# Kernel optimization log

Hardware: AMD Instinct MI355X
Metric: run time of the kernel (lower is better)

Reference implementation:

```python
import jax, jax.numpy as jnp
import numpy as np

N_NODES = 100000
N_EDGES = 1600000
IN_DIM = 64
OUT_DIM = 64
HIDDEN = 64  # fixed in edge_weight_mlp
POS_DIM = 3


def setup_inputs() -> dict:
    key = jax.random.key(0)
    ks = jax.random.split(key, 10)
    x = jax.random.normal(ks[0], (N_NODES, IN_DIM), dtype=jnp.float32)
    edge_index = jax.random.randint(ks[1], (2, N_EDGES), 0, N_NODES, dtype=jnp.int64)
    pos = jax.random.normal(ks[2], (N_NODES, POS_DIM), dtype=jnp.float32)
    # edge_weight_mlp params: Linear(2*IN_DIM+1 -> 64), Linear(64 -> 1)
    s1 = 1.0 / np.sqrt(2 * IN_DIM + 1)
    w1 = jax.random.uniform(ks[3], (2 * IN_DIM + 1, HIDDEN), jnp.float32, -s1, s1)
    b1 = jax.random.uniform(ks[4], (HIDDEN,), jnp.float32, -s1, s1)
    s2 = 1.0 / np.sqrt(HIDDEN)
    w2 = jax.random.uniform(ks[5], (HIDDEN, 1), jnp.float32, -s2, s2)
    b2 = jax.random.uniform(ks[6], (1,), jnp.float32, -s2, s2)
    # transform: Linear(IN_DIM -> OUT_DIM)
    st = 1.0 / np.sqrt(IN_DIM)
    wt = jax.random.uniform(ks[7], (IN_DIM, OUT_DIM), jnp.float32, -st, st)
    bt = jax.random.uniform(ks[8], (OUT_DIM,), jnp.float32, -st, st)
    return {"x": x, "edge_index": edge_index, "pos": pos,
            "w1": w1, "b1": b1, "w2": w2, "b2": b2, "wt": wt, "bt": bt}


def reference(x, edge_index, pos, w1, b1, w2, b2, wt, bt):
    src, dst = edge_index[0], edge_index[1]
    # edge weights: MLP on [x_src, x_dst, |pos_dst - pos_src|]
    edge_length = jnp.linalg.norm(pos[dst] - pos[src], axis=1, keepdims=True)  # [E,1]
    edge_feat = jnp.concatenate([x[src], x[dst], edge_length], axis=1)  # [E, 2*in+1]
    h = jax.nn.relu(edge_feat @ w1 + b1)
    edge_weights = jax.nn.sigmoid(h @ w2 + b2)  # [E,1]
    # node transform, gather, weight, scatter-add
    x_t = x @ wt + bt  # [N, out]
    messages = x_t[src] * edge_weights  # [E, out]
    out = jax.ops.segment_sum(messages, dst, num_segments=x.shape[0])  # [N, out]
    return out, edge_weights
```

## Files before the change

### kernel.cpp

```cpp
#include <hip/hip_runtime.h>
#include <hip/hip_bf16.h>
#include <math.h>

#define NN 100000
#define NE 1600000
#define CAP 48
#define NB 391
#define BCAP 4608
#define EPB 4096
#define NBLKA ((NE + EPB - 1) / EPB)
#define PSTR 72

typedef __attribute__((ext_vector_type(8))) short short8;
typedef __attribute__((ext_vector_type(4))) float floatx4;

static __device__ __forceinline__ unsigned short f2bb(float f) {
    __hip_bfloat16 h = __float2bfloat16(f);
    return *(unsigned short*)&h;
}

__global__ __launch_bounds__(256) void prep_mfma(
    const float* __restrict__ x, const float* __restrict__ w1,
    const float* __restrict__ b1, const float* __restrict__ pos,
    unsigned int* __restrict__ rec, unsigned short* __restrict__ hd,
    float4* __restrict__ pos4) {
    __shared__ unsigned short As[64 * PSTR];
    __shared__ unsigned short Bs[128 * PSTR];
    int t = threadIdx.x;
    int nbase = blockIdx.x * 64;
    {
        int r = t & 63;
        int node = nbase + r; if (node >= NN) node = NN - 1;
        const float4* xr = (const float4*)(x + (size_t)node * 64);
#pragma unroll
        for (int i = 0; i < 4; ++i) {
            int s = (t >> 6) + 4 * i;
            float4 v = xr[s];
            ushort4 o = {f2bb(v.x), f2bb(v.y), f2bb(v.z), f2bb(v.w)};
            *(ushort4*)&As[r * PSTR + s * 4] = o;
        }
    }
    {
        int n = t & 127;
        int kh = t >> 7;
        int krow = (n < 64) ? 0 : 64;
        int col = n & 63;
#pragma unroll
        for (int i = 0; i < 32; ++i) {
            int k = kh * 32 + i;
            Bs[n * PSTR + k] = f2bb(w1[(krow + k) * 64 + col]);
        }
    }
    if (t < 64) {
        int node = nbase + t;
        if (node < NN)
            pos4[node] = make_float4(pos[node * 3 + 0], pos[node * 3 + 1],
                                     pos[node * 3 + 2], 0.f);
    }
    __syncthreads();
    int lane = t & 63, wave = t >> 6;
    int grp = lane >> 4, l15 = lane & 15;
    floatx4 acc[8] = {};
    int arow = wave * 16 + l15;
#pragma unroll
    for (int ks = 0; ks < 2; ++ks) {
        int koff = ks * 32 + grp * 8;
        short8 a = *(const short8*)&As[arow * PSTR + koff];
#pragma unroll
        for (int nt = 0; nt < 8; ++nt) {
            short8 b = *(const short8*)&Bs[(nt * 16 + l15) * PSTR + koff];
            acc[nt] = __builtin_amdgcn_mfma_f32_16x16x32_bf16(a, b, acc[nt], 0, 0, 0);
        }
    }
#pragma unroll
    for (int nt = 0; nt < 8; ++nt) {
#pragma unroll
        for (int r = 0; r < 4; ++r) {
            int nr = wave * 16 + grp * 4 + r;
            int node = nbase + nr;
            if (node >= NN) continue;
            if (nt < 4) {
                int col = nt * 16 + l15;
                unsigned xbits = As[nr * PSTR + col];
                rec[(size_t)node * 64 + col] =
                    ((unsigned)f2bb(acc[nt][r]) << 16) | xbits;
            } else {
                int col = (nt - 4) * 16 + l15;
                hd[(size_t)node * 64 + col] = f2bb(acc[nt][r] + b1[col]);
            }
        }
    }
}

__global__ __launch_bounds__(256) void bucket_kernel(
    const int* __restrict__ ei, int* __restrict__ gcursor,
    uint2* __restrict__ bucketed) {
    __shared__ int cnt[NB];
    __shared__ int base_s[NB];
    int t = threadIdx.x;
    for (int i = t; i < NB; i += 256) cnt[i] = 0;
    __syncthreads();
    int e0 = blockIdx.x * EPB;
    unsigned int tags[16];
    int srcs[16], dsts[16];
#pragma unroll
    for (int i = 0; i < 16; ++i) {
        int e = e0 + i * 256 + t;
        tags[i] = 0xFFFFFFFFu;
        if (e < NE) {
            srcs[i] = ei[e];
            dsts[i] = ei[NE + e];
            int b = dsts[i] >> 8;
            int slot = atomicAdd(&cnt[b], 1);
            tags[i] = ((unsigned)b << 12) | (unsigned)slot;
        }
    }
    __syncthreads();
    for (int b = t; b < NB; b += 256)
        base_s[b] = atomicAdd(&gcursor[b], cnt[b]);
    __syncthreads();
#pragma unroll
    for (int i = 0; i < 16; ++i) {
        if (tags[i] != 0xFFFFFFFFu) {
            int e = e0 + i * 256 + t;
            int b = (int)(tags[i] >> 12);
            int slot = (int)(tags[i] & 0xFFFu);
            int pos = base_s[b] + slot;
            if (pos < BCAP) {
                bucketed[(size_t)b * BCAP + pos] =
                    make_uint2((unsigned)srcs[i] | (((unsigned)dsts[i] & 255u) << 17),
                               (unsigned)e);
            }
        }
    }
}

__global__ __launch_bounds__(1024) void csr_kernel(
    const uint2* __restrict__ bucketed, const int* __restrict__ gcursor,
    uint2* __restrict__ pairs, int* __restrict__ deg) {
    __shared__ int cur[256];
    int t = threadIdx.x;
    if (t < 256) cur[t] = 0;
    __syncthreads();
    int b = blockIdx.x;
    int n0 = b << 8;
    int cnt = gcursor[b];
    if (cnt > BCAP) cnt = BCAP;
    for (int i = t; i < cnt; i += 1024) {
        uint2 en = bucketed[(size_t)b * BCAP + i];
        int dwb = (int)((en.x >> 17) & 255u);
        unsigned src = en.x & 0x1FFFFu;
        int slot = atomicAdd(&cur[dwb], 1);
        if (slot < CAP)
            pairs[(size_t)(n0 + dwb) * CAP + slot] = make_uint2(src, en.y);
    }
    __syncthreads();
    if (t < 256) {
        int node = n0 + t;
        if (node < NN) deg[node] = (cur[t] > CAP) ? CAP : cur[t];
    }
}

__global__ __launch_bounds__(256) void mega_kernel(
    const uint2* __restrict__ pairs, const int* __restrict__ deg,
    const unsigned int* __restrict__ rec, const unsigned short* __restrict__ hd,
    const float4* __restrict__ pos4, const float* __restrict__ w1,
    const float* __restrict__ w2, const float* __restrict__ b2,
    float* __restrict__ ew_out, unsigned short* __restrict__ aggb,
    float* __restrict__ sumw) {
    int t = threadIdx.x;
    int w = t >> 6, lane = t & 63;
    int e4 = lane >> 4, hg = lane & 15;
    int node = blockIdx.x * 4 + w;
    if (node >= NN) return;

    float acc0 = 0.f, acc1 = 0.f, acc2 = 0.f, acc3 = 0.f, sw = 0.f;
    int d = deg[node];
    uint2 hz = ((const uint2*)(hd + (size_t)node * 64))[hg];
    float zb0 = __uint_as_float(hz.x << 16);
    float zb1 = __uint_as_float(hz.x & 0xFFFF0000u);
    float zb2 = __uint_as_float(hz.y << 16);
    float zb3 = __uint_as_float(hz.y & 0xFFFF0000u);
    float4 w24 = ((const float4*)w2)[hg];
    float4 wl4 = ((const float4*)(w1 + 128 * 64))[hg];
    float4 pd = pos4[node];
    float b2v = b2[0];
    const uint2* seg = pairs + (size_t)node * CAP;

    if (d > 0) {
        int i0 = (e4 < d) ? e4 : (d - 1);
        uint2 pr_c = seg[i0];
        int i1 = (4 + e4 < d) ? (4 + e4) : (d - 1);
        uint2 pr_n = (4 < d) ? seg[i1] : pr_c;
        uint4 u_c = ((const uint4*)rec)[(size_t)pr_c.x * 16 + hg];
        float4 ps_c = pos4[pr_c.x];

        for (int j = 0; j < d; j += 4) {
            int jn = j + 4;
            uint2 pr_n2 = pr_n;
            uint4 u_n = u_c;
            float4 ps_n = ps_c;
            if (jn < d) {
                u_n = ((const uint4*)rec)[(size_t)pr_n.x * 16 + hg];
                ps_n = pos4[pr_n.x];
                int i2 = (jn + 4 + e4 < d) ? (jn + 4 + e4) : (d - 1);
                if (jn + 4 < d) pr_n2 = seg[i2];
            }
            bool valid = (j + e4 < d);
            float dx = pd.x - ps_c.x;
            float dy = pd.y - ps_c.y;
            float dz = pd.z - ps_c.z;
            float len = __builtin_amdgcn_sqrtf(dx * dx + dy * dy + dz * dz);

            float z0 = zb0 + __uint_as_float(u_c.x & 0xFFFF0000u) + len * wl4.x;
            float z1 = zb1 + __uint_as_float(u_c.y & 0xFFFF0000u) + len * wl4.y;
            float z2 = zb2 + __uint_as_float(u_c.z & 0xFFFF0000u) + len * wl4.z;
            float z3 = zb3 + __uint_as_float(u_c.w & 0xFFFF0000u) + len * wl4.w;
            float tt = fmaxf(z0, 0.f) * w24.x;
            tt = fmaf(fmaxf(z1, 0.f), w24.y, tt);
            tt = fmaf(fmaxf(z2, 0.f), w24.z, tt);
            tt = fmaf(fmaxf(z3, 0.f), w24.w, tt);
            tt += __shfl_xor(tt, 1);
            tt += __shfl_xor(tt, 2);
            tt += __shfl_xor(tt, 4);
            tt += __shfl_xor(tt, 8);
            float ew = __builtin_amdgcn_rcpf(1.f + __expf(-(tt + b2v)));
            if (valid) {
                if (hg == 0) ew_out[pr_c.y] = ew;
                acc0 = fmaf(ew, __uint_as_float(u_c.x << 16), acc0);
                acc1 = fmaf(ew, __uint_as_float(u_c.y << 16), acc1);
                acc2 = fmaf(ew, __uint_as_float(u_c.z << 16), acc2);
                acc3 = fmaf(ew, __uint_as_float(u_c.w << 16), acc3);
                sw += ew;
            }
            pr_c = pr_n; pr_n = pr_n2; u_c = u_n; ps_c = ps_n;
        }
    }
#pragma unroll
    for (int off = 16; off < 64; off <<= 1) {
        acc0 += __shfl_xor(acc0, off);
        acc1 += __shfl_xor(acc1, off);
        acc2 += __shfl_xor(acc2, off);
        acc3 += __shfl_xor(acc3, off);
        sw   += __shfl_xor(sw, off);
    }
    if (e4 == 0) {
        ushort4 o = {f2bb(acc0), f2bb(acc1), f2bb(acc2), f2bb(acc3)};
        *(ushort4*)(aggb + (size_t)node * 64 + hg * 4) = o;
    }
    if (lane == 0) sumw[node] = sw;
}

__global__ __launch_bounds__(256) void transform_mfma(
    const unsigned short* __restrict__ aggb, const float* __restrict__ sumw,
    const float* __restrict__ wt, const float* __restrict__ bt,
    float* __restrict__ out) {
    __shared__ unsigned short As[64 * PSTR];
    __shared__ unsigned short Bs[64 * PSTR];
    int t = threadIdx.x;
    int nbase = blockIdx.x * 64;
    {
        int r = t & 63;
        int node = nbase + r; if (node >= NN) node = NN - 1;
        const uint4* ar = (const uint4*)(aggb + (size_t)node * 64);
#pragma unroll
        for (int i = 0; i < 2; ++i) {
            int s = (t >> 6) + 4 * i;
            *(uint4*)&As[r * PSTR + s * 8] = ar[s];
        }
    }
    {
        int n = t & 63;
        int kq = t >> 6;
#pragma unroll
        for (int i = 0; i < 16; ++i) {
            int k = kq * 16 + i;
            Bs[n * PSTR + k] = f2bb(wt[k * 64 + n]);
        }
    }
    __syncthreads();
    int lane = t & 63, wave = t >> 6;
    int grp = lane >> 4, l15 = lane & 15;
    floatx4 acc[4] = {};
    int arow = wave * 16 + l15;
#pragma unroll
    for (int ks = 0; ks < 2; ++ks) {
        int koff = ks * 32 + grp * 8;
        short8 a = *(const short8*)&As[arow * PSTR + koff];
#pragma unroll
        for (int nt = 0; nt < 4; ++nt) {
            short8 b = *(const short8*)&Bs[(nt * 16 + l15) * PSTR + koff];
            acc[nt] = __builtin_amdgcn_mfma_f32_16x16x32_bf16(a, b, acc[nt], 0, 0, 0);
        }
    }
#pragma unroll
    for (int nt = 0; nt < 4; ++nt) {
        int col = nt * 16 + l15;
        float btv = bt[col];
#pragma unroll
        for (int r = 0; r < 4; ++r) {
            int node = nbase + wave * 16 + grp * 4 + r;
            if (node < NN)
                out[(size_t)node * 64 + col] = acc[nt][r] + sumw[node] * btv;
        }
    }
}

extern "C" void kernel_launch(void* const* d_in, const int* in_sizes, int n_in,
                              void* d_out, int out_size, void* d_ws, size_t ws_size,
                              hipStream_t stream) {
    const float* x   = (const float*)d_in[0];
    const int*   ei  = (const int*)d_in[1];
    const float* pos = (const float*)d_in[2];
    const float* w1  = (const float*)d_in[3];
    const float* b1  = (const float*)d_in[4];
    const float* w2  = (const float*)d_in[5];
    const float* b2  = (const float*)d_in[6];
    const float* wt  = (const float*)d_in[7];
    const float* bt  = (const float*)d_in[8];

    float* out    = (float*)d_out;
    float* ew_out = out + (size_t)NN * 64;

    unsigned int* rec = (unsigned int*)d_ws;
    unsigned short* hd = (unsigned short*)(rec + (size_t)NN * 64);
    uint2* pairs = (uint2*)(hd + (size_t)NN * 64);
    unsigned short* aggb = (unsigned short*)(pairs + (size_t)NN * CAP);
    float4* pos4 = (float4*)(aggb + (size_t)NN * 64);
    float* sumw = (float*)(pos4 + NN);
    int* gcursor = (int*)(sumw + NN);
    int* deg = gcursor + NB;

    uint2* bucketed = (uint2*)d_out;

    hipMemsetAsync(gcursor, 0, NB * sizeof(int), stream);
    prep_mfma<<<(NN + 63) / 64, 256, 0, stream>>>(x, w1, b1, pos, rec, hd, pos4);
    bucket_kernel<<<NBLKA, 256, 0, stream>>>(ei, gcursor, bucketed);
    csr_kernel<<<NB, 1024, 0, stream>>>(bucketed, gcursor, pairs, deg);
    mega_kernel<<<(NN + 3) / 4, 256, 0, stream>>>(pairs, deg, rec, hd, pos4,
                                                  w1, w2, b2, ew_out, aggb, sumw);
    transform_mfma<<<(NN + 63) / 64, 256, 0, stream>>>(aggb, sumw, wt, bt, out);
}
```

Baseline: 259.3 us.

## Fuse prep and bucket kernels; process 8 edges per wave in mega kernel

Merges the node-prep MFMA kernel and the edge-bucketing kernel into one launch, with block index choosing the role and a shared LDS buffer, so the two independent phases can overlap and one launch is removed. Separately, the mega kernel now handles 8 edges per wave step with 8 lanes per edge, each lane owning 8 features. This halves the loop trip count and cuts one shuffle stage from the per-edge reduction. The cost is more registers per lane, and lanes go idle when a node's degree is not a multiple of 8.

```diff
diff --git a/kernel.cpp b/kernel.cpp
--- a/kernel.cpp
+++ b/kernel.cpp
@@ -9,6 +9,7 @@
 #define BCAP 4608
 #define EPB 4096
 #define NBLKA ((NE + EPB - 1) / EPB)
+#define NPREP ((NN + 63) / 64)
 #define PSTR 72
 
 typedef __attribute__((ext_vector_type(8))) short short8;
@@ -18,118 +19,125 @@
     __hip_bfloat16 h = __float2bfloat16(f);
     return *(unsigned short*)&h;
 }
-
-__global__ __launch_bounds__(256) void prep_mfma(
+static __device__ __forceinline__ float hi_f(unsigned u) {
+    return __uint_as_float(u & 0xFFFF0000u);
+}
+static __device__ __forceinline__ float lo_f(unsigned u) {
+    return __uint_as_float(u << 16);
+}
+
+__global__ __launch_bounds__(256) void fused_prep_bucket(
     const float* __restrict__ x, const float* __restrict__ w1,
     const float* __restrict__ b1, const float* __restrict__ pos,
+    const int* __restrict__ ei,
     unsigned int* __restrict__ rec, unsigned short* __restrict__ hd,
-    float4* __restrict__ pos4) {
-    __shared__ unsigned short As[64 * PSTR];
-    __shared__ unsigned short Bs[128 * PSTR];
+    float4* __restrict__ pos4, int* __restrict__ gcursor,
+    uint2* __restrict__ bucketed) {
+    __shared__ __align__(16) unsigned char smem[(64 + 128) * PSTR * 2];
     int t = threadIdx.x;
-    int nbase = blockIdx.x * 64;
-    {
-        int r = t & 63;
-        int node = nbase + r; if (node >= NN) node = NN - 1;
-        const float4* xr = (const float4*)(x + (size_t)node * 64);
-#pragma unroll
-        for (int i = 0; i < 4; ++i) {
-            int s = (t >> 6) + 4 * i;
-            float4 v = xr[s];
-            ushort4 o = {f2bb(v.x), f2bb(v.y), f2bb(v.z), f2bb(v.w)};
-            *(ushort4*)&As[r * PSTR + s * 4] = o;
-        }
-    }
-    {
-        int n = t & 127;
-        int kh = t >> 7;
-        int krow = (n < 64) ? 0 : 64;
-        int col = n & 63;
-#pragma unroll
-        for (int i = 0; i < 32; ++i) {
-            int k = kh * 32 + i;
-            Bs[n * PSTR + k] = f2bb(w1[(krow + k) * 64 + col]);
-        }
-    }
-    if (t < 64) {
-        int node = nbase + t;
-        if (node < NN)
-            pos4[node] = make_float4(pos[node * 3 + 0], pos[node * 3 + 1],
-                                     pos[node * 3 + 2], 0.f);
-    }
-    __syncthreads();
-    int lane = t & 63, wave = t >> 6;
-    int grp = lane >> 4, l15 = lane & 15;
-    floatx4 acc[8] = {};
-    int arow = wave * 16 + l15;
-#pragma unroll
-    for (int ks = 0; ks < 2; ++ks) {
-        int koff = ks * 32 + grp * 8;
-        short8 a = *(const short8*)&As[arow * PSTR + koff];
+    if (blockIdx.x < NPREP) {
+        unsigned short* As = (unsigned short*)smem;
+        unsigned short* Bs = As + 64 * PSTR;
+        int nbase = blockIdx.x * 64;
+        {
+            int r = t & 63;
+            int node = nbase + r; if (node >= NN) node = NN - 1;
+            const float4* xr = (const float4*)(x + (size_t)node * 64);
+#pragma unroll
+            for (int i = 0; i < 4; ++i) {
+                int s = (t >> 6) + 4 * i;
+                float4 v = xr[s];
+                ushort4 o = {f2bb(v.x), f2bb(v.y), f2bb(v.z), f2bb(v.w)};
+                *(ushort4*)&As[r * PSTR + s * 4] = o;
+            }
+        }
+        {
+            int n = t & 127;
+            int kh = t >> 7;
+            int krow = (n < 64) ? 0 : 64;
+            int col = n & 63;
+#pragma unroll
+            for (int i = 0; i < 32; ++i) {
+                int k = kh * 32 + i;
+                Bs[n * PSTR + k] = f2bb(w1[(krow + k) * 64 + col]);
+            }
+        }
+        if (t < 64) {
+            int node = nbase + t;
+            if (node < NN)
+                pos4[node] = make_float4(pos[node * 3 + 0], pos[node * 3 + 1],
+                                         pos[node * 3 + 2], 0.f);
+        }
+        __syncthreads();
+        int lane = t & 63, wave = t >> 6;
+        int grp = lane >> 4, l15 = lane & 15;
+        floatx4 acc[8] = {};
+        int arow = wave * 16 + l15;
+#pragma unroll
+        for (int ks = 0; ks < 2; ++ks) {
+            int koff = ks * 32 + grp * 8;
+            short8 a = *(const short8*)&As[arow * PSTR + koff];
+#pragma unroll
+            for (int nt = 0; nt < 8; ++nt) {
+                short8 b = *(const short8*)&Bs[(nt * 16 + l15) * PSTR + koff];
+                acc[nt] = __builtin_amdgcn_mfma_f32_16x16x32_bf16(a, b, acc[nt], 0, 0, 0);
+            }
+        }
 #pragma unroll
         for (int nt = 0; nt < 8; ++nt) {
-            short8 b = *(const short8*)&Bs[(nt * 16 + l15) * PSTR + koff];
-            acc[nt] = __builtin_amdgcn_mfma_f32_16x16x32_bf16(a, b, acc[nt], 0, 0, 0);
-        }
-    }
-#pragma unroll
-    for (int nt = 0; nt < 8; ++nt) {
-#pragma unroll
-        for (int r = 0; r < 4; ++r) {
-            int nr = wave * 16 + grp * 4 + r;
-            int node = nbase + nr;
-            if (node >= NN) continue;
-            if (nt < 4) {
-                int col = nt * 16 + l15;
-                unsigned xbits = As[nr * PSTR + col];
-                rec[(size_t)node * 64 + col] =
-                    ((unsigned)f2bb(acc[nt][r]) << 16) | xbits;
-            } else {
-                int col = (nt - 4) * 16 + l15;
-                hd[(size_t)node * 64 + col] = f2bb(acc[nt][r] + b1[col]);
-            }
-        }
-    }
-}
-
-__global__ __launch_bounds__(256) void bucket_kernel(
-    const int* __restrict__ ei, int* __restrict__ gcursor,
-    uint2* __restrict__ bucketed) {
-    __shared__ int cnt[NB];
-    __shared__ int base_s[NB];
-    int t = threadIdx.x;
-    for (int i = t; i < NB; i += 256) cnt[i] = 0;
-    __syncthreads();
-    int e0 = blockIdx.x * EPB;
-    unsigned int tags[16];
-    int srcs[16], dsts[16];
-#pragma unroll
-    for (int i = 0; i < 16; ++i) {
-        int e = e0 + i * 256 + t;
-        tags[i] = 0xFFFFFFFFu;
-        if (e < NE) {
-            srcs[i] = ei[e];
-            dsts[i] = ei[NE + e];
-            int b = dsts[i] >> 8;
-            int slot = atomicAdd(&cnt[b], 1);
-            tags[i] = ((unsigned)b << 12) | (unsigned)slot;
-        }
-    }
-    __syncthreads();
-    for (int b = t; b < NB; b += 256)
-        base_s[b] = atomicAdd(&gcursor[b], cnt[b]);
-    __syncthreads();
-#pragma unroll
-    for (int i = 0; i < 16; ++i) {
-        if (tags[i] != 0xFFFFFFFFu) {
+#pragma unroll
+            for (int r = 0; r < 4; ++r) {
+                int nr = wave * 16 + grp * 4 + r;
+                int node = nbase + nr;
+                if (node >= NN) continue;
+                if (nt < 4) {
+                    int col = nt * 16 + l15;
+                    unsigned xbits = As[nr * PSTR + col];
+                    rec[(size_t)node * 64 + col] =
+                        ((unsigned)f2bb(acc[nt][r]) << 16) | xbits;
+                } else {
+                    int col = (nt - 4) * 16 + l15;
+                    hd[(size_t)node * 64 + col] = f2bb(acc[nt][r] + b1[col]);
+                }
+            }
+        }
+    } else {
+        int* cnt = (int*)smem;
+        int* base_s = cnt + NB;
+        for (int i = t; i < NB; i += 256) cnt[i] = 0;
+        __syncthreads();
+        int e0 = (blockIdx.x - NPREP) * EPB;
+        unsigned int tags[16];
+        int srcs[16], dsts[16];
+#pragma unroll
+        for (int i = 0; i < 16; ++i) {
             int e = e0 + i * 256 + t;
-            int b = (int)(tags[i] >> 12);
-            int slot = (int)(tags[i] & 0xFFFu);
-            int pos = base_s[b] + slot;
-            if (pos < BCAP) {
-                bucketed[(size_t)b * BCAP + pos] =
-                    make_uint2((unsigned)srcs[i] | (((unsigned)dsts[i] & 255u) << 17),
-                               (unsigned)e);
+            tags[i] = 0xFFFFFFFFu;
+            if (e < NE) {
+                srcs[i] = ei[e];
+                dsts[i] = ei[NE + e];
+                int b = dsts[i] >> 8;
+                int slot = atomicAdd(&cnt[b], 1);
+                tags[i] = ((unsigned)b << 12) | (unsigned)slot;
+            }
+        }
+        __syncthreads();
+        for (int b = t; b < NB; b += 256)
+            base_s[b] = atomicAdd(&gcursor[b], cnt[b]);
+        __syncthreads();
+#pragma unroll
+        for (int i = 0; i < 16; ++i) {
+            if (tags[i] != 0xFFFFFFFFu) {
+                int e = e0 + i * 256 + t;
+                int b = (int)(tags[i] >> 12);
+                int slot = (int)(tags[i] & 0xFFFu);
+                int p = base_s[b] + slot;
+                if (p < BCAP) {
+                    bucketed[(size_t)b * BCAP + p] =
+                        make_uint2((unsigned)srcs[i] |
+                                   (((unsigned)dsts[i] & 255u) << 17),
+                                   (unsigned)e);
+                }
             }
         }
     }
@@ -170,83 +178,114 @@
     float* __restrict__ sumw) {
     int t = threadIdx.x;
     int w = t >> 6, lane = t & 63;
-    int e4 = lane >> 4, hg = lane & 15;
+    int e8 = lane >> 3, hg = lane & 7;
     int node = blockIdx.x * 4 + w;
     if (node >= NN) return;
 
-    float acc0 = 0.f, acc1 = 0.f, acc2 = 0.f, acc3 = 0.f, sw = 0.f;
+    float acc0 = 0.f, acc1 = 0.f, acc2 = 0.f, acc3 = 0.f;
+    float acc4 = 0.f, acc5 = 0.f, acc6 = 0.f, acc7 = 0.f, sw = 0.f;
     int d = deg[node];
-    uint2 hz = ((const uint2*)(hd + (size_t)node * 64))[hg];
-    float zb0 = __uint_as_float(hz.x << 16);
-    float zb1 = __uint_as_float(hz.x & 0xFFFF0000u);
-    float zb2 = __uint_as_float(hz.y << 16);
-    float zb3 = __uint_as_float(hz.y & 0xFFFF0000u);
-    float4 w24 = ((const float4*)w2)[hg];
-    float4 wl4 = ((const float4*)(w1 + 128 * 64))[hg];
+    uint4 hz = ((const uint4*)(hd + (size_t)node * 64))[hg];
+    float zb0 = lo_f(hz.x), zb1 = hi_f(hz.x);
+    float zb2 = lo_f(hz.y), zb3 = hi_f(hz.y);
+    float zb4 = lo_f(hz.z), zb5 = hi_f(hz.z);
+    float zb6 = lo_f(hz.w), zb7 = hi_f(hz.w);
+    float4 w2a = ((const float4*)w2)[2 * hg];
+    float4 w2b = ((const float4*)w2)[2 * hg + 1];
+    float4 wla = ((const float4*)(w1 + 128 * 64))[2 * hg];
+    float4 wlb = ((const float4*)(w1 + 128 * 64))[2 * hg + 1];
     float4 pd = pos4[node];
     float b2v = b2[0];
     const uint2* seg = pairs + (size_t)node * CAP;
+    const uint4* rec4 = (const uint4*)rec;
 
     if (d > 0) {
-        int i0 = (e4 < d) ? e4 : (d - 1);
+        int i0 = (e8 < d) ? e8 : (d - 1);
         uint2 pr_c = seg[i0];
-        int i1 = (4 + e4 < d) ? (4 + e4) : (d - 1);
-        uint2 pr_n = (4 < d) ? seg[i1] : pr_c;
-        uint4 u_c = ((const uint4*)rec)[(size_t)pr_c.x * 16 + hg];
+        uint2 pr_n = pr_c;
+        if (8 < d) { int i1 = (8 + e8 < d) ? (8 + e8) : (d - 1); pr_n = seg[i1]; }
+        uint4 ua_c = rec4[(size_t)pr_c.x * 16 + 2 * hg];
+        uint4 ub_c = rec4[(size_t)pr_c.x * 16 + 2 * hg + 1];
         float4 ps_c = pos4[pr_c.x];
 
-        for (int j = 0; j < d; j += 4) {
-            int jn = j + 4;
+        for (int j = 0; j < d; j += 8) {
+            int jn = j + 8;
             uint2 pr_n2 = pr_n;
-            uint4 u_n = u_c;
+            uint4 ua_n = ua_c, ub_n = ub_c;
             float4 ps_n = ps_c;
             if (jn < d) {
-                u_n = ((const uint4*)rec)[(size_t)pr_n.x * 16 + hg];
+                ua_n = rec4[(size_t)pr_n.x * 16 + 2 * hg];
+                ub_n = rec4[(size_t)pr_n.x * 16 + 2 * hg + 1];
                 ps_n = pos4[pr_n.x];
-                int i2 = (jn + 4 + e4 < d) ? (jn + 4 + e4) : (d - 1);
-                if (jn + 4 < d) pr_n2 = seg[i2];
-            }
-            bool valid = (j + e4 < d);
+                if (jn + 8 < d) {
+                    int i2 = (jn + 8 + e8 < d) ? (jn + 8 + e8) : (d - 1);
+                    pr_n2 = seg[i2];
+                }
+            }
+            bool valid = (j + e8 < d);
             float dx = pd.x - ps_c.x;
             float dy = pd.y - ps_c.y;
             float dz = pd.z - ps_c.z;
             float len = __builtin_amdgcn_sqrtf(dx * dx + dy * dy + dz * dz);
 
-            float z0 = zb0 + __uint_as_float(u_c.x & 0xFFFF0000u) + len * wl4.x;
-            float z1 = zb1 + __uint_as_float(u_c.y & 0xFFFF0000u) + len * wl4.y;
-            float z2 = zb2 + __uint_as_float(u_c.z & 0xFFFF0000u) + len * wl4.z;
-            float z3 = zb3 + __uint_as_float(u_c.w & 0xFFFF0000u) + len * wl4.w;
-            float tt = fmaxf(z0, 0.f) * w24.x;
-            tt = fmaf(fmaxf(z1, 0.f), w24.y, tt);
-            tt = fmaf(fmaxf(z2, 0.f), w24.z, tt);
-            tt = fmaf(fmaxf(z3, 0.f), w24.w, tt);
+            float tt;
+            {
+                float z0 = zb0 + hi_f(ua_c.x) + len * wla.x;
+                float z1 = zb1 + hi_f(ua_c.y) + len * wla.y;
+                float z2 = zb2 + hi_f(ua_c.z) + len * wla.z;
+                float z3 = zb3 + hi_f(ua_c.w) + len * wla.w;
+                float z4 = zb4 + hi_f(ub_c.x) + len * wlb.x;
+                float z5 = zb5 + hi_f(ub_c.y) + len * wlb.y;
+                float z6 = zb6 + hi_f(ub_c.z) + len * wlb.z;
+                float z7 = zb7 + hi_f(ub_c.w) + len * wlb.w;
+                tt = fmaxf(z0, 0.f) * w2a.x;
+                tt = fmaf(fmaxf(z1, 0.f), w2a.y, tt);
+                tt = fmaf(fmaxf(z2, 0.f), w2a.z, tt);
+                tt = fmaf(fmaxf(z3, 0.f), w2a.w, tt);
+                tt = fmaf(fmaxf(z4, 0.f), w2b.x, tt);
+                tt = fmaf(fmaxf(z5, 0.f), w2b.y, tt);
+                tt = fmaf(fmaxf(z6, 0.f), w2b.z, tt);
+                tt = fmaf(fmaxf(z7, 0.f), w2b.w, tt);
+            }
             tt += __shfl_xor(tt, 1);
             tt += __shfl_xor(tt, 2);
             tt += __shfl_xor(tt, 4);
-            tt += __shfl_xor(tt, 8);
             float ew = __builtin_amdgcn_rcpf(1.f + __expf(-(tt + b2v)));
             if (valid) {
                 if (hg == 0) ew_out[pr_c.y] = ew;
-                acc0 = fmaf(ew, __uint_as_float(u_c.x << 16), acc0);
-                acc1 = fmaf(ew, __uint_as_float(u_c.y << 16), acc1);
-                acc2 = fmaf(ew, __uint_as_float(u_c.z << 16), acc2);
-                acc3 = fmaf(ew, __uint_as_float(u_c.w << 16), acc3);
+                acc0 = fmaf(ew, lo_f(ua_c.x), acc0);
+                acc1 = fmaf(ew, lo_f(ua_c.y), acc1);
+                acc2 = fmaf(ew, lo_f(ua_c.z), acc2);
+                acc3 = fmaf(ew, lo_f(ua_c.w), acc3);
+                acc4 = fmaf(ew, lo_f(ub_c.x), acc4);
+                acc5 = fmaf(ew, lo_f(ub_c.y), acc5);
+                acc6 = fmaf(ew, lo_f(ub_c.z), acc6);
+                acc7 = fmaf(ew, lo_f(ub_c.w), acc7);
                 sw += ew;
             }
-            pr_c = pr_n; pr_n = pr_n2; u_c = u_n; ps_c = ps_n;
-        }
-    }
-#pragma unroll
-    for (int off = 16; off < 64; off <<= 1) {
+            pr_c = pr_n; pr_n = pr_n2;
+            ua_c = ua_n; ub_c = ub_n; ps_c = ps_n;
+        }
+    }
+#pragma unroll
+    for (int off = 8; off < 64; off <<= 1) {
         acc0 += __shfl_xor(acc0, off);
         acc1 += __shfl_xor(acc1, off);
         acc2 += __shfl_xor(acc2, off);
         acc3 += __shfl_xor(acc3, off);
+        acc4 += __shfl_xor(acc4, off);
+        acc5 += __shfl_xor(acc5, off);
+        acc6 += __shfl_xor(acc6, off);
+        acc7 += __shfl_xor(acc7, off);
         sw   += __shfl_xor(sw, off);
     }
-    if (e4 == 0) {
-        ushort4 o = {f2bb(acc0), f2bb(acc1), f2bb(acc2), f2bb(acc3)};
-        *(ushort4*)(aggb + (size_t)node * 64 + hg * 4) = o;
+    if (e8 == 0) {
+        uint4 o;
+        o.x = ((unsigned)f2bb(acc1) << 16) | f2bb(acc0);
+        o.y = ((unsigned)f2bb(acc3) << 16) | f2bb(acc2);
+        o.z = ((unsigned)f2bb(acc5) << 16) | f2bb(acc4);
+        o.w = ((unsigned)f2bb(acc7) << 16) | f2bb(acc6);
+        *(uint4*)(aggb + (size_t)node * 64 + hg * 8) = o;
     }
     if (lane == 0) sumw[node] = sw;
 }
@@ -334,8 +373,8 @@
     uint2* bucketed = (uint2*)d_out;
 
     hipMemsetAsync(gcursor, 0, NB * sizeof(int), stream);
-    prep_mfma<<<(NN + 63) / 64, 256, 0, stream>>>(x, w1, b1, pos, rec, hd, pos4);
-    bucket_kernel<<<NBLKA, 256, 0, stream>>>(ei, gcursor, bucketed);
+    fused_prep_bucket<<<NPREP + NBLKA, 256, 0, stream>>>(
+        x, w1, b1, pos, ei, rec, hd, pos4, gcursor, bucketed);
     csr_kernel<<<NB, 1024, 0, stream>>>(bucketed, gcursor, pairs, deg);
     mega_kernel<<<(NN + 3) / 4, 256, 0, stream>>>(pairs, deg, rec, hd, pos4,
                                                   w1, w2, b2, ew_out, aggb, sumw);
```

Measured after the change: 244.7 us. -5.6%, faster.
